# Kernel tuning notes

Measured on AMD Instinct MI355X. Metric: run time of the kernel, lower is better.

Reference implementation:

```python
import jax, jax.numpy as jnp
import numpy as np

N = 50000      # nodes
E = 800000     # edges (avg degree 16)
IN_DIM = 128
HID = 64       # num_hidden
HEADS = 1
NUM_LAYERS = 3       # -> 4 SNATConv layers total
SLOPE = 0.2          # negative_slope
THR = 0.01           # threhold: edges with attention < THR are pruned after layer 0


def setup_inputs() -> dict:
    key = jax.random.key(0)
    ks = jax.random.split(key, 16)
    s = 0.05
    x = jax.random.normal(ks[0], (N, IN_DIM), jnp.float32)
    edge_src = jax.random.randint(ks[1], (E,), 0, N)
    edge_dst = jax.random.randint(ks[2], (E,), 0, N)
    W_embed = jax.random.normal(ks[3], (IN_DIM, HID), jnp.float32) * s
    n_conv = NUM_LAYERS + 1
    # all conv layers map HID*HEADS -> HEADS*HID (heads==1 so square)
    W_gat = jax.random.normal(ks[4], (n_conv, HID, HEADS * HID), jnp.float32) * s
    a_l = jax.random.normal(ks[5], (n_conv, HEADS, HID), jnp.float32) * s
    a_r = jax.random.normal(ks[6], (n_conv, HEADS, HID), jnp.float32) * s
    d_cat = (NUM_LAYERS + 1) * HID
    W0 = jax.random.normal(ks[7], (d_cat, HID), jnp.float32) * s
    b0 = jnp.zeros((HID,), jnp.float32)
    W1 = jax.random.normal(ks[8], (HID, HID), jnp.float32) * s
    b1 = jnp.zeros((HID,), jnp.float32)
    W2 = jax.random.normal(ks[9], (HID, 1), jnp.float32) * s
    b2 = jnp.zeros((1,), jnp.float32)
    return {"x": x, "edge_src": edge_src, "edge_dst": edge_dst,
            "W_embed": W_embed, "W_gat": W_gat, "a_l": a_l, "a_r": a_r,
            "W0": W0, "b0": b0, "W1": W1, "b1": b1, "W2": W2, "b2": b2}


def _edge_softmax(e, dst):
    # e: [E, H] raw scores; softmax over incoming edges of each dst node
    m = jax.ops.segment_max(e, dst, num_segments=N)       # [N, H]
    a = jnp.exp(e - m[dst])
    s = jax.ops.segment_sum(a, dst, num_segments=N)       # [N, H]
    return a / jnp.maximum(s[dst], 1e-9)


def _snat_conv(h, W, al, ar, src, dst, mask):
    # h: [N, F_in]; W: [F_in, H*HID]; al/ar: [H, HID]
    feat = (h @ W).reshape(N, HEADS, HID)                 # [N, H, HID]
    el = jnp.sum(feat * al, axis=-1)                      # [N, H]
    er = jnp.sum(feat * ar, axis=-1)
    e = jax.nn.leaky_relu(el[src] + er[dst], SLOPE)       # [E, H]
    if mask is not None:
        e = jnp.where(mask, e, -1e9)                      # prune thresholded edges
    alpha = _edge_softmax(e, dst)                         # [E, H]
    out = jax.ops.segment_sum(feat[src] * alpha[..., None], dst, num_segments=N)
    return jax.nn.elu(out), alpha                         # [N, H, HID], [E, H]


def reference(x, edge_src, edge_dst, W_embed, W_gat, a_l, a_r, W0, b0, W1, b1, W2, b2):
    src, dst = edge_src, edge_dst
    h = jnp.tanh(x @ W_embed)                             # [N, HID]
    # layer 0: computes attention and the threshold mask (index_1 / index_0)
    h0, alpha = _snat_conv(h, W_gat[0], a_l[0], a_r[0], src, dst, None)
    mask = alpha >= THR                                   # [E, H] kept-edge mask
    h = h0.reshape(N, HEADS * HID)
    H_cat = [h]
    for l in range(1, NUM_LAYERS):                        # middle layers reuse mask
        hl, _ = _snat_conv(h, W_gat[l], a_l[l], a_r[l], src, dst, mask)
        h = hl.reshape(N, HEADS * HID)
        H_cat.append(h)
    feats, _ = _snat_conv(h, W_gat[NUM_LAYERS], a_l[NUM_LAYERS], a_r[NUM_LAYERS], src, dst, mask)
    feats = feats.mean(axis=1)                            # [N, HID] mean over heads
    f = jnp.concatenate(H_cat + [feats], axis=1)          # [N, (L+1)*HID]
    out = jax.nn.relu(f @ W0 + b0)                        # activationP
    out = jax.nn.relu(out @ W1 + b1)
    out = jax.nn.relu(out @ W2 + b2)                      # final F.relu
    return out                                            # [N, 1]
```

## Files before the change

kernel.cpp:

```cpp
#include <hip/hip_runtime.h>
#include <math.h>


__global__ void k_zero(int* __restrict__ counts, int N) {
  int i = blockIdx.x * 256 + threadIdx.x;
  if (i < N) counts[i] = 0;
}

__global__ void k_hist(const int* __restrict__ dst, int* __restrict__ counts, int E) {
  int e = blockIdx.x * blockDim.x + threadIdx.x;
  if (e < E) atomicAdd(&counts[dst[e]], 1);
}

__global__ __launch_bounds__(1024) void k_bsum(const int* __restrict__ counts,
                                               int* __restrict__ bsum, int n) {
  __shared__ int wsum[16];
  int tid = threadIdx.x, lane = tid & 63, wid = tid >> 6;
  int i = blockIdx.x * 1024 + tid;
  int v = (i < n) ? counts[i] : 0;
  #pragma unroll
  for (int off = 32; off; off >>= 1) v += __shfl_xor(v, off, 64);
  if (lane == 0) wsum[wid] = v;
  __syncthreads();
  if (wid == 0) {
    int w = (lane < 16) ? wsum[lane] : 0;
    #pragma unroll
    for (int off = 8; off; off >>= 1) w += __shfl_xor(w, off, 64);
    if (lane == 0) bsum[blockIdx.x] = w;
  }
}

__global__ __launch_bounds__(64) void k_bscan(const int* __restrict__ bsum,
                                              int* __restrict__ bofs,
                                              int* __restrict__ row_ptr,
                                              int nb, int n) {
  int lane = threadIdx.x;
  int carry = 0;
  for (int base = 0; base < nb; base += 64) {
    int idx = base + lane;
    int orig = (idx < nb) ? bsum[idx] : 0;
    int inc = orig;
    #pragma unroll
    for (int off = 1; off < 64; off <<= 1) {
      int t = __shfl_up(inc, off, 64);
      if (lane >= off) inc += t;
    }
    if (idx < nb) bofs[idx] = carry + inc - orig;
    carry += __shfl(inc, 63, 64);
  }
  if (lane == 0) row_ptr[n] = carry;
}

__global__ __launch_bounds__(1024) void k_scan3(const int* __restrict__ counts,
                                                const int* __restrict__ bofs,
                                                int* __restrict__ row_ptr,
                                                int* __restrict__ cursor, int n) {
  __shared__ int wsum[16];
  int tid = threadIdx.x, lane = tid & 63, wid = tid >> 6;
  int i = blockIdx.x * 1024 + tid;
  int v = (i < n) ? counts[i] : 0;
  int inc = v;
  #pragma unroll
  for (int off = 1; off < 64; off <<= 1) {
    int t = __shfl_up(inc, off, 64);
    if (lane >= off) inc += t;
  }
  if (lane == 63) wsum[wid] = inc;
  __syncthreads();
  if (wid == 0 && lane < 16) {
    int orig = wsum[lane];
    int w = orig;
    #pragma unroll
    for (int off = 1; off < 16; off <<= 1) {
      int t = __shfl_up(w, off, 64);
      if (lane >= off) w += t;
    }
    wsum[lane] = w - orig;
  }
  __syncthreads();
  int excl = bofs[blockIdx.x] + wsum[wid] + inc - v;
  if (i < n) { row_ptr[i] = excl; cursor[i] = excl; }
}

__global__ void k_scatter(const int* __restrict__ src, const int* __restrict__ dst,
                          int* __restrict__ cursor, int* __restrict__ csr_src, int E) {
  int e = blockIdx.x * blockDim.x + threadIdx.x;
  if (e < E) {
    int pos = atomicAdd(&cursor[dst[e]], 1);
    csr_src[pos] = src[e];
  }
}

__global__ __launch_bounds__(256, 4) void k_embed_feat(
    const float* __restrict__ x, const float* __restrict__ We,
    const float* __restrict__ Wg, const float* __restrict__ al,
    const float* __restrict__ ar, float* __restrict__ feat,
    float* __restrict__ el, float* __restrict__ er, int N) {
  __shared__ float sA[64 * 129];
  __shared__ float sE[64 * 8];
  int tid = threadIdx.x, lane = tid & 63, wv = tid >> 6;
  int nb0 = blockIdx.x * 64, nl = N - 1;
  int r = tid >> 2, p = tid & 3;
  {
    const float* gp = x + (size_t)min(nb0 + r, nl) * 128;
    #pragma unroll
    for (int half = 0; half < 2; half++) {
      const float* g = gp + half * 64 + p * 16;
      float4 v0 = *(const float4*)(g + 0), v1 = *(const float4*)(g + 4);
      float4 v2 = *(const float4*)(g + 8), v3 = *(const float4*)(g + 12);
      float* dp = &sA[r * 129 + half * 64 + p * 16];
      dp[0]=v0.x; dp[1]=v0.y; dp[2]=v0.z; dp[3]=v0.w;
      dp[4]=v1.x; dp[5]=v1.y; dp[6]=v1.z; dp[7]=v1.w;
      dp[8]=v2.x; dp[9]=v2.y; dp[10]=v2.z; dp[11]=v2.w;
      dp[12]=v3.x; dp[13]=v3.y; dp[14]=v3.z; dp[15]=v3.w;
    }
  }
  __syncthreads();
  int f0 = __builtin_amdgcn_readfirstlane(wv * 16);
  float acc[16];
  #pragma unroll
  for (int f = 0; f < 16; f++) acc[f] = 0.f;
  #pragma unroll 8
  for (int k = 0; k < 128; k++) {
    float ak = sA[lane * 129 + k];
    const float* wr = We + k * 64 + f0;
    #pragma unroll
    for (int f = 0; f < 16; f++) acc[f] = fmaf(ak, wr[f], acc[f]);
  }
  __syncthreads();
  #pragma unroll
  for (int f = 0; f < 16; f++) sA[lane * 65 + f0 + f] = tanhf(acc[f]);
  __syncthreads();
  float acc2[16];
  #pragma unroll
  for (int f = 0; f < 16; f++) acc2[f] = 0.f;
  #pragma unroll 8
  for (int k = 0; k < 64; k++) {
    float ak = sA[lane * 65 + k];
    const float* wr = Wg + k * 64 + f0;
    #pragma unroll
    for (int f = 0; f < 16; f++) acc2[f] = fmaf(ak, wr[f], acc2[f]);
  }
  float rl = 0.f, rr = 0.f;
  #pragma unroll
  for (int f = 0; f < 16; f++) {
    rl = fmaf(acc2[f], al[f0 + f], rl);
    rr = fmaf(acc2[f], ar[f0 + f], rr);
  }
  sE[lane * 8 + wv] = rl;
  sE[lane * 8 + 4 + wv] = rr;
  __syncthreads();
  #pragma unroll
  for (int f = 0; f < 16; f++) sA[lane * 65 + f0 + f] = acc2[f];
  __syncthreads();
  {
    int n = nb0 + r;
    if (n < N) {
      const float* sp = &sA[r * 65 + p * 16];
      float* gp = feat + (size_t)n * 64 + p * 16;
      #pragma unroll
      for (int q = 0; q < 4; q++)
        *(float4*)(gp + q * 4) = make_float4(sp[q*4+0], sp[q*4+1], sp[q*4+2], sp[q*4+3]);
    }
  }
  if (tid < 64) {
    int n = nb0 + tid;
    if (n < N) {
      el[n] = (sE[tid*8+0] + sE[tid*8+1]) + (sE[tid*8+2] + sE[tid*8+3]);
      er[n] = (sE[tid*8+4] + sE[tid*8+5]) + (sE[tid*8+6] + sE[tid*8+7]);
    }
  }
}

__global__ __launch_bounds__(256, 4) void k_feat(const float* __restrict__ hin,
                                                 const float* __restrict__ Wg,
                                                 const float* __restrict__ al,
                                                 const float* __restrict__ ar,
                                                 float* __restrict__ feat,
                                                 float* __restrict__ el,
                                                 float* __restrict__ er, int N) {
  __shared__ float sA[64 * 65];
  __shared__ float sE[64 * 8];
  int tid = threadIdx.x, lane = tid & 63, wv = tid >> 6;
  int nb0 = blockIdx.x * 64;
  int nl = N - 1;
  int r = tid >> 2, p = tid & 3;
  {
    const float* g = hin + (size_t)min(nb0 + r, nl) * 64 + p * 16;
    float4 v0 = *(const float4*)(g + 0), v1 = *(const float4*)(g + 4);
    float4 v2 = *(const float4*)(g + 8), v3 = *(const float4*)(g + 12);
    float* dp = &sA[r * 65 + p * 16];
    dp[0]=v0.x; dp[1]=v0.y; dp[2]=v0.z; dp[3]=v0.w;
    dp[4]=v1.x; dp[5]=v1.y; dp[6]=v1.z; dp[7]=v1.w;
    dp[8]=v2.x; dp[9]=v2.y; dp[10]=v2.z; dp[11]=v2.w;
    dp[12]=v3.x; dp[13]=v3.y; dp[14]=v3.z; dp[15]=v3.w;
  }
  __syncthreads();
  int f0 = __builtin_amdgcn_readfirstlane(wv * 16);
  float acc[16];
  #pragma unroll
  for (int f = 0; f < 16; f++) acc[f] = 0.f;
  #pragma unroll 8
  for (int k = 0; k < 64; k++) {
    float ak = sA[lane * 65 + k];
    const float* wr = Wg + k * 64 + f0;
    #pragma unroll
    for (int f = 0; f < 16; f++) acc[f] = fmaf(ak, wr[f], acc[f]);
  }
  float rl = 0.f, rr = 0.f;
  #pragma unroll
  for (int f = 0; f < 16; f++) {
    rl = fmaf(acc[f], al[f0 + f], rl);
    rr = fmaf(acc[f], ar[f0 + f], rr);
  }
  __syncthreads();
  #pragma unroll
  for (int f = 0; f < 16; f++) sA[lane * 65 + f0 + f] = acc[f];
  sE[lane * 8 + wv] = rl;
  sE[lane * 8 + 4 + wv] = rr;
  __syncthreads();
  {
    int n = nb0 + r;
    if (n < N) {
      const float* sp = &sA[r * 65 + p * 16];
      float* gp = feat + (size_t)n * 64 + p * 16;
      #pragma unroll
      for (int q = 0; q < 4; q++)
        *(float4*)(gp + q * 4) = make_float4(sp[q*4+0], sp[q*4+1], sp[q*4+2], sp[q*4+3]);
    }
  }
  if (tid < 64) {
    int n = nb0 + tid;
    if (n < N) {
      el[n] = (sE[tid*8+0] + sE[tid*8+1]) + (sE[tid*8+2] + sE[tid*8+3]);
      er[n] = (sE[tid*8+4] + sE[tid*8+5]) + (sE[tid*8+6] + sE[tid*8+7]);
    }
  }
}

__global__ __launch_bounds__(256) void k_aggr(const float* __restrict__ feat,
                                              const float* __restrict__ el,
                                              const float* __restrict__ er,
                                              const int* __restrict__ row_ptr,
                                              const int* __restrict__ csr_src,
                                              unsigned char* __restrict__ mask,
                                              int write_mask, int use_mask,
                                              float* __restrict__ hout, int N) {
  __shared__ __align__(16) int   su[4][64];
  __shared__ __align__(16) float spl[4][64];
  int wv = (int)((blockIdx.x * blockDim.x + threadIdx.x) >> 6);
  int wave = threadIdx.x >> 6, lane = threadIdx.x & 63;
  if (wv >= N) return;
  int beg = row_ptr[wv], end = row_ptr[wv + 1];
  int deg = end - beg;
  float erv = er[wv];
  float acc0 = 0.f, acc1 = 0.f, acc2 = 0.f, acc3 = 0.f;
  if (deg <= 64) {
    int k = beg + lane;
    bool have = (lane < deg);
    int u = have ? csr_src[k] : 0;
    float sc = -INFINITY;
    if (have) {
      float e0 = el[u] + erv;
      sc = (e0 >= 0.f) ? e0 : 0.2f * e0;
      if (use_mask && mask[k] == 0) sc = -1e9f;
    }
    float m = sc;
    #pragma unroll
    for (int off = 32; off; off >>= 1) m = fmaxf(m, __shfl_xor(m, off, 64));
    float pl = have ? expf(sc - m) : 0.f;
    float s = pl;
    #pragma unroll
    for (int off = 32; off; off >>= 1) s += __shfl_xor(s, off, 64);
    pl *= 1.0f / fmaxf(s, 1e-9f);
    if (write_mask && have) mask[k] = (pl >= 0.01f) ? 1 : 0;
    su[wave][lane] = u;
    spl[wave][lane] = pl;
    int dq = (deg + 3) >> 2;
    #pragma unroll 2
    for (int q = 0; q < dq; q++) {
      int4   uu = *(const int4*)&su[wave][q * 4];
      float4 pp = *(const float4*)&spl[wave][q * 4];
      acc0 = fmaf(pp.x, feat[(size_t)uu.x * 64 + lane], acc0);
      acc1 = fmaf(pp.y, feat[(size_t)uu.y * 64 + lane], acc1);
      acc2 = fmaf(pp.z, feat[(size_t)uu.z * 64 + lane], acc2);
      acc3 = fmaf(pp.w, feat[(size_t)uu.w * 64 + lane], acc3);
    }
  } else {
    float m = -INFINITY, s = 0.f;
    for (int base = beg; base < end; base += 64) {
      int k = base + lane;
      float sc = -INFINITY;
      if (k < end) {
        int u = csr_src[k];
        float e0 = el[u] + erv;
        sc = (e0 >= 0.f) ? e0 : 0.2f * e0;
        if (use_mask && mask[k] == 0) sc = -1e9f;
      }
      float cm = sc;
      #pragma unroll
      for (int off = 32; off; off >>= 1) cm = fmaxf(cm, __shfl_xor(cm, off, 64));
      float nm = fmaxf(m, cm);
      float t = (k < end) ? expf(sc - nm) : 0.f;
      #pragma unroll
      for (int off = 32; off; off >>= 1) t += __shfl_xor(t, off, 64);
      s = s * expf(m - nm) + t;
      m = nm;
    }
    float inv = 1.0f / fmaxf(s, 1e-9f);
    for (int base = beg; base < end; base += 64) {
      int k = base + lane;
      int u = 0;
      float pl = 0.f;
      if (k < end) {
        u = csr_src[k];
        float e0 = el[u] + erv;
        float sc = (e0 >= 0.f) ? e0 : 0.2f * e0;
        if (use_mask && mask[k] == 0) sc = -1e9f;
        pl = expf(sc - m) * inv;
        if (write_mask) mask[k] = (pl >= 0.01f) ? 1 : 0;
      }
      su[wave][lane] = u;
      spl[wave][lane] = pl;
      int cnt = min(64, end - base);
      int dq = (cnt + 3) >> 2;
      for (int q = 0; q < dq; q++) {
        int4   uu = *(const int4*)&su[wave][q * 4];
        float4 pp = *(const float4*)&spl[wave][q * 4];
        acc0 = fmaf(pp.x, feat[(size_t)uu.x * 64 + lane], acc0);
        acc1 = fmaf(pp.y, feat[(size_t)uu.y * 64 + lane], acc1);
        acc2 = fmaf(pp.z, feat[(size_t)uu.z * 64 + lane], acc2);
        acc3 = fmaf(pp.w, feat[(size_t)uu.w * 64 + lane], acc3);
      }
    }
  }
  float acc = (acc0 + acc1) + (acc2 + acc3);
  hout[(size_t)wv * 64 + lane] = (acc > 0.f) ? acc : expm1f(acc);
}

__global__ __launch_bounds__(256, 4) void k_mlp(const float* __restrict__ o0,
                                                const float* __restrict__ o1,
                                                const float* __restrict__ o2,
                                                const float* __restrict__ o3,
                                                const float* __restrict__ W0,
                                                const float* __restrict__ b0,
                                                const float* __restrict__ W1,
                                                const float* __restrict__ b1,
                                                const float* __restrict__ W2,
                                                const float* __restrict__ b2,
                                                float* __restrict__ out, int N) {
  __shared__ float sA[64 * 65];
  __shared__ float sR[64 * 5];
  int tid = threadIdx.x, lane = tid & 63, wv = tid >> 6;
  int nb0 = blockIdx.x * 64;
  int nl = N - 1;
  int f0 = __builtin_amdgcn_readfirstlane(wv * 16);
  float acc[16];
  #pragma unroll
  for (int f = 0; f < 16; f++) acc[f] = b0[f0 + f];
  int r = tid >> 2, p = tid & 3;

  auto seg = [&](const float* __restrict__ sp, const float* __restrict__ wp) {
    __syncthreads();
    {
      const float* g = sp + (size_t)min(nb0 + r, nl) * 64 + p * 16;
      float4 v0 = *(const float4*)(g + 0), v1 = *(const float4*)(g + 4);
      float4 v2 = *(const float4*)(g + 8), v3 = *(const float4*)(g + 12);
      float* dp = &sA[r * 65 + p * 16];
      dp[0]=v0.x; dp[1]=v0.y; dp[2]=v0.z; dp[3]=v0.w;
      dp[4]=v1.x; dp[5]=v1.y; dp[6]=v1.z; dp[7]=v1.w;
      dp[8]=v2.x; dp[9]=v2.y; dp[10]=v2.z; dp[11]=v2.w;
      dp[12]=v3.x; dp[13]=v3.y; dp[14]=v3.z; dp[15]=v3.w;
    }
    __syncthreads();
    #pragma unroll 8
    for (int k = 0; k < 64; k++) {
      float ak = sA[lane * 65 + k];
      const float* wr = wp + k * 64 + f0;
      #pragma unroll
      for (int f = 0; f < 16; f++) acc[f] = fmaf(ak, wr[f], acc[f]);
    }
  };
  seg(o0, W0);
  seg(o1, W0 + 64 * 64);
  seg(o2, W0 + 128 * 64);
  seg(o3, W0 + 192 * 64);

  __syncthreads();
  #pragma unroll
  for (int f = 0; f < 16; f++)
    sA[lane * 65 + f0 + f] = (acc[f] > 0.f) ? acc[f] : 0.f;
  __syncthreads();
  float a1[16];
  #pragma unroll
  for (int f = 0; f < 16; f++) a1[f] = b1[f0 + f];
  #pragma unroll 8
  for (int k = 0; k < 64; k++) {
    float ak = sA[lane * 65 + k];
    const float* wr = W1 + k * 64 + f0;
    #pragma unroll
    for (int f = 0; f < 16; f++) a1[f] = fmaf(ak, wr[f], a1[f]);
  }
  float rp = 0.f;
  #pragma unroll
  for (int f = 0; f < 16; f++) {
    float t = (a1[f] > 0.f) ? a1[f] : 0.f;
    rp = fmaf(t, W2[f0 + f], rp);
  }
  sR[lane * 5 + wv] = rp;
  __syncthreads();
  if (tid < 64) {
    int n = nb0 + tid;
    if (n < N) {
      float o = (sR[tid*5+0] + sR[tid*5+1]) + (sR[tid*5+2] + sR[tid*5+3]) + b2[0];
      out[n] = (o > 0.f) ? o : 0.f;
    }
  }
}

extern "C" void kernel_launch(void* const* d_in, const int* in_sizes, int n_in,
                              void* d_out, int out_size, void* d_ws, size_t ws_size,
                              hipStream_t stream) {
  const float* x       = (const float*)d_in[0];
  const int*   esrc    = (const int*)d_in[1];
  const int*   edst    = (const int*)d_in[2];
  const float* W_embed = (const float*)d_in[3];
  const float* W_gat   = (const float*)d_in[4];
  const float* a_l     = (const float*)d_in[5];
  const float* a_r     = (const float*)d_in[6];
  const float* W0      = (const float*)d_in[7];
  const float* b0      = (const float*)d_in[8];
  const float* W1      = (const float*)d_in[9];
  const float* b1      = (const float*)d_in[10];
  const float* W2      = (const float*)d_in[11];
  const float* b2      = (const float*)d_in[12];
  float* out = (float*)d_out;
  const int N = in_sizes[0] / 128;
  const int E = in_sizes[1];

  char* p = (char*)d_ws;
  auto alloc = [&](size_t bytes) -> char* {
    char* r = p;
    p += (bytes + 255) & ~(size_t)255;
    return r;
  };
  float* out0 = (float*)alloc((size_t)N * 64 * 4);
  float* out1 = (float*)alloc((size_t)N * 64 * 4);
  float* out2 = (float*)alloc((size_t)N * 64 * 4);
  float* out3 = (float*)alloc((size_t)N * 64 * 4);
  float* feat = (float*)alloc((size_t)N * 64 * 4);
  float* el   = (float*)alloc((size_t)N * 4);
  float* er   = (float*)alloc((size_t)N * 4);
  int* counts  = (int*)alloc((size_t)N * 4);
  int* row_ptr = (int*)alloc((size_t)(N + 1) * 4);
  int* cursor  = (int*)alloc((size_t)N * 4);
  int* csr_src = (int*)alloc((size_t)E * 4);
  unsigned char* mask = (unsigned char*)alloc((size_t)E);
  int nb = (N + 1023) / 1024;
  int* bsum = (int*)alloc((size_t)nb * 4);
  int* bofs = (int*)alloc((size_t)nb * 4);

  k_zero<<<(N + 255) / 256, 256, 0, stream>>>(counts, N);
  k_hist<<<(E + 255) / 256, 256, 0, stream>>>(edst, counts, E);
  k_bsum<<<nb, 1024, 0, stream>>>(counts, bsum, N);
  k_bscan<<<1, 64, 0, stream>>>(bsum, bofs, row_ptr, nb, N);
  k_scan3<<<nb, 1024, 0, stream>>>(counts, bofs, row_ptr, cursor, N);
  k_scatter<<<(E + 255) / 256, 256, 0, stream>>>(esrc, edst, cursor, csr_src, E);

  int dgb = (N + 63) / 64;

  k_embed_feat<<<dgb, 256, 0, stream>>>(x, W_embed, W_gat,
                                        a_l, a_r, feat, el, er, N);
  float* outs[4] = {out0, out1, out2, out3};
  k_aggr<<<(N + 3) / 4, 256, 0, stream>>>(feat, el, er, row_ptr, csr_src, mask,
                                          1, 0, out0, N);

  for (int l = 1; l < 4; l++) {
    k_feat<<<dgb, 256, 0, stream>>>(outs[l - 1], W_gat + (size_t)l * 4096,
                                    a_l + (size_t)l * 64, a_r + (size_t)l * 64,
                                    feat, el, er, N);
    k_aggr<<<(N + 3) / 4, 256, 0, stream>>>(feat, el, er, row_ptr, csr_src, mask,
                                            0, 1, outs[l], N);
  }

  k_mlp<<<dgb, 256, 0, stream>>>(out0, out1, out2, out3, W0, b0,
                                 W1, b1, W2, b2, out, N);
}
```

Before: 453.2 us.

## Restructure dense GEMM kernels: stage weights in LDS, split K across half-waves

The feature-transform, embed and MLP kernels now stage each 64x64 weight block in LDS instead of reading weights from global memory per FMA. Each lane reads its node rows straight from global memory into registers, and the K dimension is split between the two half-waves. Each lane computes two nodes over half of K, and the halves are combined with a cross-lane shuffle. This is meant to replace scalar global weight loads and row-wise LDS staging with vectorised LDS weight reads and more register reuse. The cost is higher register pressure from two 16-wide accumulators and extra shuffles.

```diff
diff --git a/kernel.cpp b/kernel.cpp
--- a/kernel.cpp
+++ b/kernel.cpp
@@ -91,86 +91,39 @@
   }
 }
 
-__global__ __launch_bounds__(256, 4) void k_embed_feat(
-    const float* __restrict__ x, const float* __restrict__ We,
-    const float* __restrict__ Wg, const float* __restrict__ al,
-    const float* __restrict__ ar, float* __restrict__ feat,
-    float* __restrict__ el, float* __restrict__ er, int N) {
-  __shared__ float sA[64 * 129];
-  __shared__ float sE[64 * 8];
-  int tid = threadIdx.x, lane = tid & 63, wv = tid >> 6;
-  int nb0 = blockIdx.x * 64, nl = N - 1;
-  int r = tid >> 2, p = tid & 3;
-  {
-    const float* gp = x + (size_t)min(nb0 + r, nl) * 128;
-    #pragma unroll
-    for (int half = 0; half < 2; half++) {
-      const float* g = gp + half * 64 + p * 16;
-      float4 v0 = *(const float4*)(g + 0), v1 = *(const float4*)(g + 4);
-      float4 v2 = *(const float4*)(g + 8), v3 = *(const float4*)(g + 12);
-      float* dp = &sA[r * 129 + half * 64 + p * 16];
-      dp[0]=v0.x; dp[1]=v0.y; dp[2]=v0.z; dp[3]=v0.w;
-      dp[4]=v1.x; dp[5]=v1.y; dp[6]=v1.z; dp[7]=v1.w;
-      dp[8]=v2.x; dp[9]=v2.y; dp[10]=v2.z; dp[11]=v2.w;
-      dp[12]=v3.x; dp[13]=v3.y; dp[14]=v3.z; dp[15]=v3.w;
-    }
-  }
-  __syncthreads();
-  int f0 = __builtin_amdgcn_readfirstlane(wv * 16);
-  float acc[16];
-  #pragma unroll
-  for (int f = 0; f < 16; f++) acc[f] = 0.f;
-  #pragma unroll 8
-  for (int k = 0; k < 128; k++) {
-    float ak = sA[lane * 129 + k];
-    const float* wr = We + k * 64 + f0;
-    #pragma unroll
-    for (int f = 0; f < 16; f++) acc[f] = fmaf(ak, wr[f], acc[f]);
-  }
-  __syncthreads();
-  #pragma unroll
-  for (int f = 0; f < 16; f++) sA[lane * 65 + f0 + f] = tanhf(acc[f]);
-  __syncthreads();
-  float acc2[16];
-  #pragma unroll
-  for (int f = 0; f < 16; f++) acc2[f] = 0.f;
-  #pragma unroll 8
-  for (int k = 0; k < 64; k++) {
-    float ak = sA[lane * 65 + k];
-    const float* wr = Wg + k * 64 + f0;
-    #pragma unroll
-    for (int f = 0; f < 16; f++) acc2[f] = fmaf(ak, wr[f], acc2[f]);
-  }
-  float rl = 0.f, rr = 0.f;
-  #pragma unroll
-  for (int f = 0; f < 16; f++) {
-    rl = fmaf(acc2[f], al[f0 + f], rl);
-    rr = fmaf(acc2[f], ar[f0 + f], rr);
-  }
-  sE[lane * 8 + wv] = rl;
-  sE[lane * 8 + 4 + wv] = rr;
-  __syncthreads();
-  #pragma unroll
-  for (int f = 0; f < 16; f++) sA[lane * 65 + f0 + f] = acc2[f];
-  __syncthreads();
-  {
-    int n = nb0 + r;
-    if (n < N) {
-      const float* sp = &sA[r * 65 + p * 16];
-      float* gp = feat + (size_t)n * 64 + p * 16;
-      #pragma unroll
-      for (int q = 0; q < 4; q++)
-        *(float4*)(gp + q * 4) = make_float4(sp[q*4+0], sp[q*4+1], sp[q*4+2], sp[q*4+3]);
-    }
-  }
-  if (tid < 64) {
-    int n = nb0 + tid;
-    if (n < N) {
-      el[n] = (sE[tid*8+0] + sE[tid*8+1]) + (sE[tid*8+2] + sE[tid*8+3]);
-      er[n] = (sE[tid*8+4] + sE[tid*8+5]) + (sE[tid*8+6] + sE[tid*8+7]);
-    }
-  }
-}
+#define SW_STRIDE 68
+
+#define STAGE_W(DST, SRC)                                            \
+  {                                                                  \
+    int k_ = threadIdx.x >> 2, p_ = threadIdx.x & 3;                 \
+    const float* s_ = (SRC) + k_ * 64 + p_ * 16;                     \
+    float* d_ = (DST) + k_ * SW_STRIDE + p_ * 16;                    \
+    _Pragma("unroll")                                                \
+    for (int c_ = 0; c_ < 4; c_++)                                   \
+      *(float4*)(d_ + c_ * 4) = *(const float4*)(s_ + c_ * 4);       \
+  }
+
+#define LOAD16(A, P)                                                 \
+  { _Pragma("unroll")                                                \
+    for (int c_ = 0; c_ < 4; c_++)                                   \
+      *(float4*)&(A)[c_ * 4] = *(const float4*)((P) + c_ * 4); }
+
+#define KROUND(ACC, A0, A1, KB)                                      \
+  { _Pragma("unroll")                                                \
+    for (int kk_ = 0; kk_ < 16; kk_++) {                             \
+      float w_[16];                                                  \
+      const float* wr_ = &sW[((KB) + kk_) * SW_STRIDE + f0];         \
+      LOAD16(w_, wr_);                                               \
+      _Pragma("unroll")                                              \
+      for (int j_ = 0; j_ < 16; j_++) {                              \
+        ACC[0][j_] = fmaf((A0)[kk_], w_[j_], ACC[0][j_]);            \
+        ACC[1][j_] = fmaf((A1)[kk_], w_[j_], ACC[1][j_]);            \
+      }                                                              \
+    } }
+
+#define HCOMBINE(ACC, J)                                             \
+  (((h == 0) ? ACC[0][J] : ACC[1][J]) +                              \
+   __shfl_xor((h == 0) ? ACC[1][J] : ACC[0][J], 32, 64))
 
 __global__ __launch_bounds__(256, 4) void k_feat(const float* __restrict__ hin,
                                                  const float* __restrict__ Wg,
@@ -179,61 +132,173 @@
                                                  float* __restrict__ feat,
                                                  float* __restrict__ el,
                                                  float* __restrict__ er, int N) {
-  __shared__ float sA[64 * 65];
-  __shared__ float sE[64 * 8];
+  __shared__ float sW[64 * SW_STRIDE];
+  __shared__ float sEl[512], sEr[512];
   int tid = threadIdx.x, lane = tid & 63, wv = tid >> 6;
-  int nb0 = blockIdx.x * 64;
-  int nl = N - 1;
-  int r = tid >> 2, p = tid & 3;
-  {
-    const float* g = hin + (size_t)min(nb0 + r, nl) * 64 + p * 16;
-    float4 v0 = *(const float4*)(g + 0), v1 = *(const float4*)(g + 4);
-    float4 v2 = *(const float4*)(g + 8), v3 = *(const float4*)(g + 12);
-    float* dp = &sA[r * 65 + p * 16];
-    dp[0]=v0.x; dp[1]=v0.y; dp[2]=v0.z; dp[3]=v0.w;
-    dp[4]=v1.x; dp[5]=v1.y; dp[6]=v1.z; dp[7]=v1.w;
-    dp[8]=v2.x; dp[9]=v2.y; dp[10]=v2.z; dp[11]=v2.w;
-    dp[12]=v3.x; dp[13]=v3.y; dp[14]=v3.z; dp[15]=v3.w;
-  }
-  __syncthreads();
-  int f0 = __builtin_amdgcn_readfirstlane(wv * 16);
-  float acc[16];
-  #pragma unroll
-  for (int f = 0; f < 16; f++) acc[f] = 0.f;
-  #pragma unroll 8
-  for (int k = 0; k < 64; k++) {
-    float ak = sA[lane * 65 + k];
-    const float* wr = Wg + k * 64 + f0;
-    #pragma unroll
-    for (int f = 0; f < 16; f++) acc[f] = fmaf(ak, wr[f], acc[f]);
-  }
-  float rl = 0.f, rr = 0.f;
-  #pragma unroll
-  for (int f = 0; f < 16; f++) {
-    rl = fmaf(acc[f], al[f0 + f], rl);
-    rr = fmaf(acc[f], ar[f0 + f], rr);
-  }
-  __syncthreads();
-  #pragma unroll
-  for (int f = 0; f < 16; f++) sA[lane * 65 + f0 + f] = acc[f];
-  sE[lane * 8 + wv] = rl;
-  sE[lane * 8 + 4 + wv] = rr;
-  __syncthreads();
-  {
-    int n = nb0 + r;
-    if (n < N) {
-      const float* sp = &sA[r * 65 + p * 16];
-      float* gp = feat + (size_t)n * 64 + p * 16;
-      #pragma unroll
-      for (int q = 0; q < 4; q++)
-        *(float4*)(gp + q * 4) = make_float4(sp[q*4+0], sp[q*4+1], sp[q*4+2], sp[q*4+3]);
-    }
-  }
+  int g = lane & 31, h = lane >> 5;
+  int f0 = wv * 16;
+  int nb0 = blockIdx.x * 64, nl = N - 1;
+  int n0 = nb0 + g * 2;
+  const float* p0 = hin + (size_t)min(n0, nl) * 64 + h * 32;
+  const float* p1 = hin + (size_t)min(n0 + 1, nl) * 64 + h * 32;
+  STAGE_W(sW, Wg);
+  __syncthreads();
+  float acc[2][16];
+  #pragma unroll
+  for (int j = 0; j < 16; j++) { acc[0][j] = 0.f; acc[1][j] = 0.f; }
+  {
+    float a0[16], a1[16], a2[16], a3[16];
+    LOAD16(a0, p0); LOAD16(a1, p1);
+    LOAD16(a2, p0 + 16); LOAD16(a3, p1 + 16);
+    KROUND(acc, a0, a1, h * 32);
+    KROUND(acc, a2, a3, h * 32 + 16);
+  }
+  {
+    float alv[16], arv[16];
+    LOAD16(alv, al + f0); LOAD16(arv, ar + f0);
+    float pl0 = 0.f, pl1 = 0.f, pr0 = 0.f, pr1 = 0.f;
+    #pragma unroll
+    for (int j = 0; j < 16; j++) {
+      pl0 = fmaf(acc[0][j], alv[j], pl0);
+      pl1 = fmaf(acc[1][j], alv[j], pl1);
+      pr0 = fmaf(acc[0][j], arv[j], pr0);
+      pr1 = fmaf(acc[1][j], arv[j], pr1);
+    }
+    sEl[wv * 128 + g * 4 + h]     = pl0;
+    sEl[wv * 128 + g * 4 + 2 + h] = pl1;
+    sEr[wv * 128 + g * 4 + h]     = pr0;
+    sEr[wv * 128 + g * 4 + 2 + h] = pr1;
+  }
+  float fullv[16];
+  #pragma unroll
+  for (int j = 0; j < 16; j++) fullv[j] = HCOMBINE(acc, j);
+  int node = nb0 + g * 2 + h;
+  if (node < N) {
+    float* fp = feat + (size_t)node * 64 + f0;
+    #pragma unroll
+    for (int c = 0; c < 4; c++)
+      *(float4*)(fp + c * 4) =
+          make_float4(fullv[c*4], fullv[c*4+1], fullv[c*4+2], fullv[c*4+3]);
+  }
+  __syncthreads();
   if (tid < 64) {
     int n = nb0 + tid;
     if (n < N) {
-      el[n] = (sE[tid*8+0] + sE[tid*8+1]) + (sE[tid*8+2] + sE[tid*8+3]);
-      er[n] = (sE[tid*8+4] + sE[tid*8+5]) + (sE[tid*8+6] + sE[tid*8+7]);
+      float s = 0.f;
+      #pragma unroll
+      for (int w2 = 0; w2 < 4; w2++)
+        s += sEl[w2 * 128 + tid * 2] + sEl[w2 * 128 + tid * 2 + 1];
+      el[n] = s;
+    }
+  } else if (tid < 128) {
+    int t = tid - 64, n = nb0 + t;
+    if (n < N) {
+      float s = 0.f;
+      #pragma unroll
+      for (int w2 = 0; w2 < 4; w2++)
+        s += sEr[w2 * 128 + t * 2] + sEr[w2 * 128 + t * 2 + 1];
+      er[n] = s;
+    }
+  }
+}
+
+__global__ __launch_bounds__(256, 4) void k_embed_feat(
+    const float* __restrict__ x, const float* __restrict__ We,
+    const float* __restrict__ Wg, const float* __restrict__ al,
+    const float* __restrict__ ar, float* __restrict__ feat,
+    float* __restrict__ el, float* __restrict__ er, int N) {
+  __shared__ float sW[64 * SW_STRIDE];
+  __shared__ float sH[64 * SW_STRIDE];
+  __shared__ float sEl[512], sEr[512];
+  int tid = threadIdx.x, lane = tid & 63, wv = tid >> 6;
+  int g = lane & 31, h = lane >> 5;
+  int f0 = wv * 16;
+  int nb0 = blockIdx.x * 64, nl = N - 1;
+  int n0 = nb0 + g * 2;
+  const float* x0 = x + (size_t)min(n0, nl) * 128 + h * 32;
+  const float* x1 = x + (size_t)min(n0 + 1, nl) * 128 + h * 32;
+  float acc[2][16];
+  #pragma unroll
+  for (int j = 0; j < 16; j++) { acc[0][j] = 0.f; acc[1][j] = 0.f; }
+  #pragma unroll
+  for (int R = 0; R < 2; R++) {
+    if (R) __syncthreads();
+    STAGE_W(sW, We + R * 4096);
+    __syncthreads();
+    const float* q0 = x0 + R * 64;
+    const float* q1 = x1 + R * 64;
+    float a0[16], a1[16], a2[16], a3[16];
+    LOAD16(a0, q0); LOAD16(a1, q1);
+    LOAD16(a2, q0 + 16); LOAD16(a3, q1 + 16);
+    KROUND(acc, a0, a1, h * 32);
+    KROUND(acc, a2, a3, h * 32 + 16);
+  }
+  __syncthreads();
+  STAGE_W(sW, Wg);
+  {
+    int nodeL = g * 2 + h;
+    #pragma unroll
+    for (int j = 0; j < 16; j++)
+      sH[nodeL * SW_STRIDE + f0 + j] = tanhf(HCOMBINE(acc, j));
+  }
+  __syncthreads();
+  float acc2[2][16];
+  #pragma unroll
+  for (int j = 0; j < 16; j++) { acc2[0][j] = 0.f; acc2[1][j] = 0.f; }
+  {
+    const float* r0 = &sH[(g * 2) * SW_STRIDE + h * 32];
+    const float* r1 = &sH[(g * 2 + 1) * SW_STRIDE + h * 32];
+    float a0[16], a1[16], a2[16], a3[16];
+    LOAD16(a0, r0); LOAD16(a1, r1);
+    LOAD16(a2, r0 + 16); LOAD16(a3, r1 + 16);
+    KROUND(acc2, a0, a1, h * 32);
+    KROUND(acc2, a2, a3, h * 32 + 16);
+  }
+  {
+    float alv[16], arv[16];
+    LOAD16(alv, al + f0); LOAD16(arv, ar + f0);
+    float pl0 = 0.f, pl1 = 0.f, pr0 = 0.f, pr1 = 0.f;
+    #pragma unroll
+    for (int j = 0; j < 16; j++) {
+      pl0 = fmaf(acc2[0][j], alv[j], pl0);
+      pl1 = fmaf(acc2[1][j], alv[j], pl1);
+      pr0 = fmaf(acc2[0][j], arv[j], pr0);
+      pr1 = fmaf(acc2[1][j], arv[j], pr1);
+    }
+    sEl[wv * 128 + g * 4 + h]     = pl0;
+    sEl[wv * 128 + g * 4 + 2 + h] = pl1;
+    sEr[wv * 128 + g * 4 + h]     = pr0;
+    sEr[wv * 128 + g * 4 + 2 + h] = pr1;
+  }
+  float fullv[16];
+  #pragma unroll
+  for (int j = 0; j < 16; j++) fullv[j] = HCOMBINE(acc2, j);
+  int node = nb0 + g * 2 + h;
+  if (node < N) {
+    float* fp = feat + (size_t)node * 64 + f0;
+    #pragma unroll
+    for (int c = 0; c < 4; c++)
+      *(float4*)(fp + c * 4) =
+          make_float4(fullv[c*4], fullv[c*4+1], fullv[c*4+2], fullv[c*4+3]);
+  }
+  __syncthreads();
+  if (tid < 64) {
+    int n = nb0 + tid;
+    if (n < N) {
+      float s = 0.f;
+      #pragma unroll
+      for (int w2 = 0; w2 < 4; w2++)
+        s += sEl[w2 * 128 + tid * 2] + sEl[w2 * 128 + tid * 2 + 1];
+      el[n] = s;
+    }
+  } else if (tid < 128) {
+    int t = tid - 64, n = nb0 + t;
+    if (n < N) {
+      float s = 0.f;
+      #pragma unroll
+      for (int w2 = 0; w2 < 4; w2++)
+        s += sEr[w2 * 128 + t * 2] + sEr[w2 * 128 + t * 2 + 1];
+      er[n] = s;
     }
   }
 }
@@ -278,9 +343,9 @@
     spl[wave][lane] = pl;
     int dq = (deg + 3) >> 2;
     #pragma unroll 2
-    for (int q = 0; q < dq; q++) {
-      int4   uu = *(const int4*)&su[wave][q * 4];
-      float4 pp = *(const float4*)&spl[wave][q * 4];
+    for (int qq = 0; qq < dq; qq++) {
+      int4   uu = *(const int4*)&su[wave][qq * 4];
+      float4 pp = *(const float4*)&spl[wave][qq * 4];
       acc0 = fmaf(pp.x, feat[(size_t)uu.x * 64 + lane], acc0);
       acc1 = fmaf(pp.y, feat[(size_t)uu.y * 64 + lane], acc1);
       acc2 = fmaf(pp.z, feat[(size_t)uu.z * 64 + lane], acc2);
@@ -324,9 +389,9 @@
       spl[wave][lane] = pl;
       int cnt = min(64, end - base);
       int dq = (cnt + 3) >> 2;
-      for (int q = 0; q < dq; q++) {
-        int4   uu = *(const int4*)&su[wave][q * 4];
-        float4 pp = *(const float4*)&spl[wave][q * 4];
+      for (int qq = 0; qq < dq; qq++) {
+        int4   uu = *(const int4*)&su[wave][qq * 4];
+        float4 pp = *(const float4*)&spl[wave][qq * 4];
         acc0 = fmaf(pp.x, feat[(size_t)uu.x * 64 + lane], acc0);
         acc1 = fmaf(pp.y, feat[(size_t)uu.y * 64 + lane], acc1);
         acc2 = fmaf(pp.z, feat[(size_t)uu.z * 64 + lane], acc2);
@@ -349,70 +414,73 @@
                                                 const float* __restrict__ W2,
                                                 const float* __restrict__ b2,
                                                 float* __restrict__ out, int N) {
-  __shared__ float sA[64 * 65];
-  __shared__ float sR[64 * 5];
+  __shared__ float sW[64 * SW_STRIDE];
+  __shared__ float sH[64 * SW_STRIDE];
+  __shared__ float sR[256];
   int tid = threadIdx.x, lane = tid & 63, wv = tid >> 6;
-  int nb0 = blockIdx.x * 64;
-  int nl = N - 1;
-  int f0 = __builtin_amdgcn_readfirstlane(wv * 16);
-  float acc[16];
-  #pragma unroll
-  for (int f = 0; f < 16; f++) acc[f] = b0[f0 + f];
-  int r = tid >> 2, p = tid & 3;
-
-  auto seg = [&](const float* __restrict__ sp, const float* __restrict__ wp) {
+  int g = lane & 31, h = lane >> 5;
+  int f0 = wv * 16;
+  int nb0 = blockIdx.x * 64, nl = N - 1;
+  int n0 = nb0 + g * 2;
+  float acc[2][16];
+  #pragma unroll
+  for (int j = 0; j < 16; j++) { acc[0][j] = 0.f; acc[1][j] = 0.f; }
+  const float* segs[4] = {o0, o1, o2, o3};
+  #pragma unroll
+  for (int s = 0; s < 4; s++) {
+    if (s) __syncthreads();
+    STAGE_W(sW, W0 + s * 4096);
     __syncthreads();
-    {
-      const float* g = sp + (size_t)min(nb0 + r, nl) * 64 + p * 16;
-      float4 v0 = *(const float4*)(g + 0), v1 = *(const float4*)(g + 4);
-      float4 v2 = *(const float4*)(g + 8), v3 = *(const float4*)(g + 12);
-      float* dp = &sA[r * 65 + p * 16];
-      dp[0]=v0.x; dp[1]=v0.y; dp[2]=v0.z; dp[3]=v0.w;
-      dp[4]=v1.x; dp[5]=v1.y; dp[6]=v1.z; dp[7]=v1.w;
-      dp[8]=v2.x; dp[9]=v2.y; dp[10]=v2.z; dp[11]=v2.w;
-      dp[12]=v3.x; dp[13]=v3.y; dp[14]=v3.z; dp[15]=v3.w;
-    }
-    __syncthreads();
-    #pragma unroll 8
-    for (int k = 0; k < 64; k++) {
-      float ak = sA[lane * 65 + k];
-      const float* wr = wp + k * 64 + f0;
-      #pragma unroll
-      for (int f = 0; f < 16; f++) acc[f] = fmaf(ak, wr[f], acc[f]);
-    }
-  };
-  seg(o0, W0);
-  seg(o1, W0 + 64 * 64);
-  seg(o2, W0 + 128 * 64);
-  seg(o3, W0 + 192 * 64);
-
-  __syncthreads();
-  #pragma unroll
-  for (int f = 0; f < 16; f++)
-    sA[lane * 65 + f0 + f] = (acc[f] > 0.f) ? acc[f] : 0.f;
-  __syncthreads();
-  float a1[16];
-  #pragma unroll
-  for (int f = 0; f < 16; f++) a1[f] = b1[f0 + f];
-  #pragma unroll 8
-  for (int k = 0; k < 64; k++) {
-    float ak = sA[lane * 65 + k];
-    const float* wr = W1 + k * 64 + f0;
-    #pragma unroll
-    for (int f = 0; f < 16; f++) a1[f] = fmaf(ak, wr[f], a1[f]);
-  }
-  float rp = 0.f;
-  #pragma unroll
-  for (int f = 0; f < 16; f++) {
-    float t = (a1[f] > 0.f) ? a1[f] : 0.f;
-    rp = fmaf(t, W2[f0 + f], rp);
-  }
-  sR[lane * 5 + wv] = rp;
+    const float* q0 = segs[s] + (size_t)min(n0, nl) * 64 + h * 32;
+    const float* q1 = segs[s] + (size_t)min(n0 + 1, nl) * 64 + h * 32;
+    float a0[16], a1[16], a2[16], a3[16];
+    LOAD16(a0, q0); LOAD16(a1, q1);
+    LOAD16(a2, q0 + 16); LOAD16(a3, q1 + 16);
+    KROUND(acc, a0, a1, h * 32);
+    KROUND(acc, a2, a3, h * 32 + 16);
+  }
+  __syncthreads();
+  STAGE_W(sW, W1);
+  {
+    float b0v[16];
+    LOAD16(b0v, b0 + f0);
+    int nodeL = g * 2 + h;
+    #pragma unroll
+    for (int j = 0; j < 16; j++) {
+      float z = HCOMBINE(acc, j) + b0v[j];
+      sH[nodeL * SW_STRIDE + f0 + j] = (z > 0.f) ? z : 0.f;
+    }
+  }
+  __syncthreads();
+  float acc2[2][16];
+  #pragma unroll
+  for (int j = 0; j < 16; j++) { acc2[0][j] = 0.f; acc2[1][j] = 0.f; }
+  {
+    const float* r0 = &sH[(g * 2) * SW_STRIDE + h * 32];
+    const float* r1 = &sH[(g * 2 + 1) * SW_STRIDE + h * 32];
+    float a0[16], a1[16], a2[16], a3[16];
+    LOAD16(a0, r0); LOAD16(a1, r1);
+    LOAD16(a2, r0 + 16); LOAD16(a3, r1 + 16);
+    KROUND(acc2, a0, a1, h * 32);
+    KROUND(acc2, a2, a3, h * 32 + 16);
+  }
+  {
+    float b1v[16], w2v[16];
+    LOAD16(b1v, b1 + f0); LOAD16(w2v, W2 + f0);
+    float rp = 0.f;
+    #pragma unroll
+    for (int j = 0; j < 16; j++) {
+      float z = HCOMBINE(acc2, j) + b1v[j];
+      z = (z > 0.f) ? z : 0.f;
+      rp = fmaf(z, w2v[j], rp);
+    }
+    sR[wv * 64 + g * 2 + h] = rp;
+  }
   __syncthreads();
   if (tid < 64) {
     int n = nb0 + tid;
     if (n < N) {
-      float o = (sR[tid*5+0] + sR[tid*5+1]) + (sR[tid*5+2] + sR[tid*5+3]) + b2[0];
+      float o = (sR[tid] + sR[64 + tid]) + (sR[128 + tid] + sR[192 + tid]) + b2[0];
       out[n] = (o > 0.f) ? o : 0.f;
     }
   }
```

After: 570.7 us. 25.9% more time.

## Stage weights in LDS and use 4x4 register tiles in dense GEMM kernels

Applied to the files above, without the earlier changes.

The dense per-node GEMMs (embed+feat, feat, MLP) now copy each 64x64 weight tile into shared memory and compute a 4x4 register tile per thread (4 nodes by 4 features), instead of each lane holding one node and reading 16 weights per k from global memory. Each weight float4 read from LDS is now reused across four rows, which cuts global and scalar weight traffic, and the attention dot products are finished with lane shuffles. In exchange it needs more shared memory per block, so the launch-bounds occupancy hint drops from 4 to 3. It also adds extra syncs around weight staging, and the A-operand LDS reads at stride 65/129 may cause bank conflicts.

```diff
diff --git a/kernel.cpp b/kernel.cpp
--- a/kernel.cpp
+++ b/kernel.cpp
@@ -91,16 +91,57 @@
   }
 }
 
-__global__ __launch_bounds__(256, 4) void k_embed_feat(
+#define SWS 68
+
+#define STAGE_W(DST, SRC)                                            \
+  {                                                                  \
+    int k_ = threadIdx.x >> 2, p_ = threadIdx.x & 3;                 \
+    const float* s_ = (SRC) + k_ * 64 + p_ * 16;                     \
+    float* d_ = (DST) + k_ * SWS + p_ * 16;                          \
+    _Pragma("unroll")                                                \
+    for (int c_ = 0; c_ < 4; c_++)                                   \
+      *(float4*)(d_ + c_ * 4) = *(const float4*)(s_ + c_ * 4);       \
+  }
+
+#define GEMM64(ACC, ABASE, ASTRIDE, KOFF)                            \
+  { _Pragma("unroll 4")                                              \
+    for (int k_ = 0; k_ < 64; k_++) {                                \
+      float4 w4_ = *(const float4*)&sW[k_ * SWS + fq];               \
+      float a0_ = (ABASE)[(nr +  0) * (ASTRIDE) + (KOFF) + k_];      \
+      float a1_ = (ABASE)[(nr + 16) * (ASTRIDE) + (KOFF) + k_];      \
+      float a2_ = (ABASE)[(nr + 32) * (ASTRIDE) + (KOFF) + k_];      \
+      float a3_ = (ABASE)[(nr + 48) * (ASTRIDE) + (KOFF) + k_];      \
+      ACC[0][0] = fmaf(a0_, w4_.x, ACC[0][0]);                       \
+      ACC[0][1] = fmaf(a0_, w4_.y, ACC[0][1]);                       \
+      ACC[0][2] = fmaf(a0_, w4_.z, ACC[0][2]);                       \
+      ACC[0][3] = fmaf(a0_, w4_.w, ACC[0][3]);                       \
+      ACC[1][0] = fmaf(a1_, w4_.x, ACC[1][0]);                       \
+      ACC[1][1] = fmaf(a1_, w4_.y, ACC[1][1]);                       \
+      ACC[1][2] = fmaf(a1_, w4_.z, ACC[1][2]);                       \
+      ACC[1][3] = fmaf(a1_, w4_.w, ACC[1][3]);                       \
+      ACC[2][0] = fmaf(a2_, w4_.x, ACC[2][0]);                       \
+      ACC[2][1] = fmaf(a2_, w4_.y, ACC[2][1]);                       \
+      ACC[2][2] = fmaf(a2_, w4_.z, ACC[2][2]);                       \
+      ACC[2][3] = fmaf(a2_, w4_.w, ACC[2][3]);                       \
+      ACC[3][0] = fmaf(a3_, w4_.x, ACC[3][0]);                       \
+      ACC[3][1] = fmaf(a3_, w4_.y, ACC[3][1]);                       \
+      ACC[3][2] = fmaf(a3_, w4_.z, ACC[3][2]);                       \
+      ACC[3][3] = fmaf(a3_, w4_.w, ACC[3][3]);                       \
+    } }
+
+__global__ __launch_bounds__(256, 3) void k_embed_feat(
     const float* __restrict__ x, const float* __restrict__ We,
     const float* __restrict__ Wg, const float* __restrict__ al,
     const float* __restrict__ ar, float* __restrict__ feat,
     float* __restrict__ el, float* __restrict__ er, int N) {
   __shared__ float sA[64 * 129];
+  __shared__ float sW[64 * SWS];
   __shared__ float sE[64 * 8];
   int tid = threadIdx.x, lane = tid & 63, wv = tid >> 6;
   int nb0 = blockIdx.x * 64, nl = N - 1;
   int r = tid >> 2, p = tid & 3;
+  int nr = lane >> 2, fc = lane & 3;
+  int fq = wv * 16 + fc * 4;
   {
     const float* gp = x + (size_t)min(nb0 + r, nl) * 128;
     #pragma unroll
@@ -115,43 +156,58 @@
       dp[12]=v3.x; dp[13]=v3.y; dp[14]=v3.z; dp[15]=v3.w;
     }
   }
-  __syncthreads();
-  int f0 = __builtin_amdgcn_readfirstlane(wv * 16);
-  float acc[16];
-  #pragma unroll
-  for (int f = 0; f < 16; f++) acc[f] = 0.f;
-  #pragma unroll 8
-  for (int k = 0; k < 128; k++) {
-    float ak = sA[lane * 129 + k];
-    const float* wr = We + k * 64 + f0;
-    #pragma unroll
-    for (int f = 0; f < 16; f++) acc[f] = fmaf(ak, wr[f], acc[f]);
-  }
-  __syncthreads();
-  #pragma unroll
-  for (int f = 0; f < 16; f++) sA[lane * 65 + f0 + f] = tanhf(acc[f]);
-  __syncthreads();
-  float acc2[16];
-  #pragma unroll
-  for (int f = 0; f < 16; f++) acc2[f] = 0.f;
-  #pragma unroll 8
-  for (int k = 0; k < 64; k++) {
-    float ak = sA[lane * 65 + k];
-    const float* wr = Wg + k * 64 + f0;
-    #pragma unroll
-    for (int f = 0; f < 16; f++) acc2[f] = fmaf(ak, wr[f], acc2[f]);
-  }
-  float rl = 0.f, rr = 0.f;
-  #pragma unroll
-  for (int f = 0; f < 16; f++) {
-    rl = fmaf(acc2[f], al[f0 + f], rl);
-    rr = fmaf(acc2[f], ar[f0 + f], rr);
-  }
-  sE[lane * 8 + wv] = rl;
-  sE[lane * 8 + 4 + wv] = rr;
-  __syncthreads();
-  #pragma unroll
-  for (int f = 0; f < 16; f++) sA[lane * 65 + f0 + f] = acc2[f];
+  STAGE_W(sW, We);
+  __syncthreads();
+  float acc[4][4];
+  #pragma unroll
+  for (int m = 0; m < 4; m++)
+    #pragma unroll
+    for (int j = 0; j < 4; j++) acc[m][j] = 0.f;
+  GEMM64(acc, sA, 129, 0);
+  __syncthreads();
+  STAGE_W(sW, We + 4096);
+  __syncthreads();
+  GEMM64(acc, sA, 129, 64);
+  __syncthreads();
+  STAGE_W(sW, Wg);
+  #pragma unroll
+  for (int m = 0; m < 4; m++)
+    #pragma unroll
+    for (int j = 0; j < 4; j++)
+      sA[(nr + 16 * m) * 65 + fq + j] = tanhf(acc[m][j]);
+  __syncthreads();
+  float acc2[4][4];
+  #pragma unroll
+  for (int m = 0; m < 4; m++)
+    #pragma unroll
+    for (int j = 0; j < 4; j++) acc2[m][j] = 0.f;
+  GEMM64(acc2, sA, 65, 0);
+  {
+    float alv[4], arv[4];
+    *(float4*)&alv[0] = *(const float4*)(al + fq);
+    *(float4*)&arv[0] = *(const float4*)(ar + fq);
+    #pragma unroll
+    for (int m = 0; m < 4; m++) {
+      float pl = 0.f, pr = 0.f;
+      #pragma unroll
+      for (int j = 0; j < 4; j++) {
+        pl = fmaf(acc2[m][j], alv[j], pl);
+        pr = fmaf(acc2[m][j], arv[j], pr);
+      }
+      pl += __shfl_xor(pl, 1, 64); pl += __shfl_xor(pl, 2, 64);
+      pr += __shfl_xor(pr, 1, 64); pr += __shfl_xor(pr, 2, 64);
+      if (fc == 0) {
+        sE[(nr + 16 * m) * 8 + wv] = pl;
+        sE[(nr + 16 * m) * 8 + 4 + wv] = pr;
+      }
+    }
+  }
+  __syncthreads();
+  #pragma unroll
+  for (int m = 0; m < 4; m++)
+    #pragma unroll
+    for (int j = 0; j < 4; j++)
+      sA[(nr + 16 * m) * 65 + fq + j] = acc2[m][j];
   __syncthreads();
   {
     int n = nb0 + r;
@@ -172,7 +228,7 @@
   }
 }
 
-__global__ __launch_bounds__(256, 4) void k_feat(const float* __restrict__ hin,
+__global__ __launch_bounds__(256, 3) void k_feat(const float* __restrict__ hin,
                                                  const float* __restrict__ Wg,
                                                  const float* __restrict__ al,
                                                  const float* __restrict__ ar,
@@ -180,11 +236,14 @@
                                                  float* __restrict__ el,
                                                  float* __restrict__ er, int N) {
   __shared__ float sA[64 * 65];
+  __shared__ float sW[64 * SWS];
   __shared__ float sE[64 * 8];
   int tid = threadIdx.x, lane = tid & 63, wv = tid >> 6;
   int nb0 = blockIdx.x * 64;
   int nl = N - 1;
   int r = tid >> 2, p = tid & 3;
+  int nr = lane >> 2, fc = lane & 3;
+  int fq = wv * 16 + fc * 4;
   {
     const float* g = hin + (size_t)min(nb0 + r, nl) * 64 + p * 16;
     float4 v0 = *(const float4*)(g + 0), v1 = *(const float4*)(g + 4);
@@ -195,29 +254,40 @@
     dp[8]=v2.x; dp[9]=v2.y; dp[10]=v2.z; dp[11]=v2.w;
     dp[12]=v3.x; dp[13]=v3.y; dp[14]=v3.z; dp[15]=v3.w;
   }
-  __syncthreads();
-  int f0 = __builtin_amdgcn_readfirstlane(wv * 16);
-  float acc[16];
-  #pragma unroll
-  for (int f = 0; f < 16; f++) acc[f] = 0.f;
-  #pragma unroll 8
-  for (int k = 0; k < 64; k++) {
-    float ak = sA[lane * 65 + k];
-    const float* wr = Wg + k * 64 + f0;
-    #pragma unroll
-    for (int f = 0; f < 16; f++) acc[f] = fmaf(ak, wr[f], acc[f]);
-  }
-  float rl = 0.f, rr = 0.f;
-  #pragma unroll
-  for (int f = 0; f < 16; f++) {
-    rl = fmaf(acc[f], al[f0 + f], rl);
-    rr = fmaf(acc[f], ar[f0 + f], rr);
-  }
-  __syncthreads();
-  #pragma unroll
-  for (int f = 0; f < 16; f++) sA[lane * 65 + f0 + f] = acc[f];
-  sE[lane * 8 + wv] = rl;
-  sE[lane * 8 + 4 + wv] = rr;
+  STAGE_W(sW, Wg);
+  __syncthreads();
+  float acc[4][4];
+  #pragma unroll
+  for (int m = 0; m < 4; m++)
+    #pragma unroll
+    for (int j = 0; j < 4; j++) acc[m][j] = 0.f;
+  GEMM64(acc, sA, 65, 0);
+  {
+    float alv[4], arv[4];
+    *(float4*)&alv[0] = *(const float4*)(al + fq);
+    *(float4*)&arv[0] = *(const float4*)(ar + fq);
+    #pragma unroll
+    for (int m = 0; m < 4; m++) {
+      float pl = 0.f, pr = 0.f;
+      #pragma unroll
+      for (int j = 0; j < 4; j++) {
+        pl = fmaf(acc[m][j], alv[j], pl);
+        pr = fmaf(acc[m][j], arv[j], pr);
+      }
+      pl += __shfl_xor(pl, 1, 64); pl += __shfl_xor(pl, 2, 64);
+      pr += __shfl_xor(pr, 1, 64); pr += __shfl_xor(pr, 2, 64);
+      if (fc == 0) {
+        sE[(nr + 16 * m) * 8 + wv] = pl;
+        sE[(nr + 16 * m) * 8 + 4 + wv] = pr;
+      }
+    }
+  }
+  __syncthreads();
+  #pragma unroll
+  for (int m = 0; m < 4; m++)
+    #pragma unroll
+    for (int j = 0; j < 4; j++)
+      sA[(nr + 16 * m) * 65 + fq + j] = acc[m][j];
   __syncthreads();
   {
     int n = nb0 + r;
@@ -338,7 +408,7 @@
   hout[(size_t)wv * 64 + lane] = (acc > 0.f) ? acc : expm1f(acc);
 }
 
-__global__ __launch_bounds__(256, 4) void k_mlp(const float* __restrict__ o0,
+__global__ __launch_bounds__(256, 3) void k_mlp(const float* __restrict__ o0,
                                                 const float* __restrict__ o1,
                                                 const float* __restrict__ o2,
                                                 const float* __restrict__ o3,
@@ -350,15 +420,23 @@
                                                 const float* __restrict__ b2,
                                                 float* __restrict__ out, int N) {
   __shared__ float sA[64 * 65];
+  __shared__ float sW[64 * SWS];
   __shared__ float sR[64 * 5];
   int tid = threadIdx.x, lane = tid & 63, wv = tid >> 6;
   int nb0 = blockIdx.x * 64;
   int nl = N - 1;
-  int f0 = __builtin_amdgcn_readfirstlane(wv * 16);
-  float acc[16];
-  #pragma unroll
-  for (int f = 0; f < 16; f++) acc[f] = b0[f0 + f];
   int r = tid >> 2, p = tid & 3;
+  int nr = lane >> 2, fc = lane & 3;
+  int fq = wv * 16 + fc * 4;
+  float acc[4][4];
+  {
+    float4 b0v = *(const float4*)(b0 + fq);
+    #pragma unroll
+    for (int m = 0; m < 4; m++) {
+      acc[m][0] = b0v.x; acc[m][1] = b0v.y;
+      acc[m][2] = b0v.z; acc[m][3] = b0v.w;
+    }
+  }
 
   auto seg = [&](const float* __restrict__ sp, const float* __restrict__ wp) {
     __syncthreads();
@@ -372,14 +450,9 @@
       dp[8]=v2.x; dp[9]=v2.y; dp[10]=v2.z; dp[11]=v2.w;
       dp[12]=v3.x; dp[13]=v3.y; dp[14]=v3.z; dp[15]=v3.w;
     }
+    STAGE_W(sW, wp);
     __syncthreads();
-    #pragma unroll 8
-    for (int k = 0; k < 64; k++) {
-      float ak = sA[lane * 65 + k];
-      const float* wr = wp + k * 64 + f0;
-      #pragma unroll
-      for (int f = 0; f < 16; f++) acc[f] = fmaf(ak, wr[f], acc[f]);
-    }
+    GEMM64(acc, sA, 65, 0);
   };
   seg(o0, W0);
   seg(o1, W0 + 64 * 64);
@@ -387,27 +460,40 @@
   seg(o3, W0 + 192 * 64);
 
   __syncthreads();
-  #pragma unroll
-  for (int f = 0; f < 16; f++)
-    sA[lane * 65 + f0 + f] = (acc[f] > 0.f) ? acc[f] : 0.f;
-  __syncthreads();
-  float a1[16];
-  #pragma unroll
-  for (int f = 0; f < 16; f++) a1[f] = b1[f0 + f];
-  #pragma unroll 8
-  for (int k = 0; k < 64; k++) {
-    float ak = sA[lane * 65 + k];
-    const float* wr = W1 + k * 64 + f0;
-    #pragma unroll
-    for (int f = 0; f < 16; f++) a1[f] = fmaf(ak, wr[f], a1[f]);
-  }
-  float rp = 0.f;
-  #pragma unroll
-  for (int f = 0; f < 16; f++) {
-    float t = (a1[f] > 0.f) ? a1[f] : 0.f;
-    rp = fmaf(t, W2[f0 + f], rp);
-  }
-  sR[lane * 5 + wv] = rp;
+  STAGE_W(sW, W1);
+  #pragma unroll
+  for (int m = 0; m < 4; m++)
+    #pragma unroll
+    for (int j = 0; j < 4; j++) {
+      float z = acc[m][j];
+      sA[(nr + 16 * m) * 65 + fq + j] = (z > 0.f) ? z : 0.f;
+    }
+  __syncthreads();
+  float a1[4][4];
+  {
+    float4 b1v = *(const float4*)(b1 + fq);
+    #pragma unroll
+    for (int m = 0; m < 4; m++) {
+      a1[m][0] = b1v.x; a1[m][1] = b1v.y;
+      a1[m][2] = b1v.z; a1[m][3] = b1v.w;
+    }
+  }
+  GEMM64(a1, sA, 65, 0);
+  {
+    float4 w2v = *(const float4*)(W2 + fq);
+    float w2a[4] = {w2v.x, w2v.y, w2v.z, w2v.w};
+    #pragma unroll
+    for (int m = 0; m < 4; m++) {
+      float rp = 0.f;
+      #pragma unroll
+      for (int j = 0; j < 4; j++) {
+        float t = (a1[m][j] > 0.f) ? a1[m][j] : 0.f;
+        rp = fmaf(t, w2a[j], rp);
+      }
+      rp += __shfl_xor(rp, 1, 64); rp += __shfl_xor(rp, 2, 64);
+      if (fc == 0) sR[(nr + 16 * m) * 5 + wv] = rp;
+    }
+  }
   __syncthreads();
   if (tid < 64) {
     int n = nb0 + tid;
```

Measured after the change: 452.6 us. About the same (-0.1%).
